# Kernel tuning notes

Measured on AMD Instinct MI355X. Metric: run time of the kernel, lower is better.

Reference implementation:

```python
import jax, jax.numpy as jnp
import numpy as np

N_NODES = 50000
N_EDGES = 800000
F_NODE = 64
F_EDGE = 32
F_GLOBAL = 32
OUT_DIM = 64
N_GRAPHS = 256


def setup_inputs() -> dict:
    key = jax.random.key(0)
    ks = jax.random.split(key, 8)
    x = jax.random.normal(ks[0], (N_NODES, F_NODE), dtype=jnp.float32)
    edge_index = jax.random.randint(ks[1], (2, N_EDGES), 0, N_NODES, dtype=jnp.int64)
    edge_attr = jax.random.normal(ks[2], (N_EDGES, F_EDGE), dtype=jnp.float32)
    u = jax.random.normal(ks[3], (N_GRAPHS, F_GLOBAL), dtype=jnp.float32)
    batch = jnp.sort(jax.random.randint(ks[4], (N_NODES,), 0, N_GRAPHS, dtype=jnp.int64))
    # params (scaled like default Linear init)
    W1 = jax.random.normal(ks[5], (F_NODE + F_EDGE, OUT_DIM), dtype=jnp.float32) / np.sqrt(F_NODE + F_EDGE)
    b1 = jnp.zeros((OUT_DIM,), dtype=jnp.float32)
    W2 = jax.random.normal(ks[6], (F_NODE + OUT_DIM + F_GLOBAL, OUT_DIM), dtype=jnp.float32) / np.sqrt(F_NODE + OUT_DIM + F_GLOBAL)
    b2 = jnp.zeros((OUT_DIM,), dtype=jnp.float32)
    return {"x": x, "edge_index": edge_index, "edge_attr": edge_attr,
            "u": u, "batch": batch, "W1": W1, "b1": b1, "W2": W2, "b2": b2}


def reference(x, edge_index, edge_attr, u, batch, W1, b1, W2, b2):
    dest, src = edge_index[0], edge_index[1]
    # gather source node features + edge attrs -> [E, F_NODE + F_EDGE]
    edge_info = jnp.concatenate([x[src], edge_attr], axis=1)
    # node_mlp_1: Linear + ReLU
    edge_messages = jax.nn.relu(edge_info @ W1 + b1)  # [E, OUT_DIM]
    # scatter-sum into destination nodes
    aggregated = jax.ops.segment_sum(edge_messages, dest, num_segments=x.shape[0])  # [N, OUT_DIM]
    # concat node, aggregated messages, per-graph global
    node_info = jnp.concatenate([x, aggregated, u[batch]], axis=1)  # [N, F_NODE+OUT_DIM+F_GLOBAL]
    # node_mlp_2: Linear + ReLU
    return jax.nn.relu(node_info @ W2 + b2)  # [N, OUT_DIM]
```

## Files before the change

### kernel.cpp

```cpp
#include <hip/hip_runtime.h>
#include <hip/hip_bf16.h>

typedef __attribute__((ext_vector_type(8))) short short8;
typedef __attribute__((ext_vector_type(4))) float f32x4;

constexpr int NN = 50000;
constexpr int NE = 800000;
constexpr int FN = 64;
constexpr int FE = 32;
constexpr int FG = 32;
constexpr int OD = 64;
constexpr int NG = 256;

constexpr int SCAN_B = 256;
constexpr int NBLK = (NN + SCAN_B - 1) / SCAN_B;

constexpr int SLOTS_MAX = NE + 15 * NN;
constexpr int NWIN_MAX  = SLOTS_MAX / 16;

constexpr int XCVT_BLOCKS = (NN * FN / 8 + 255) / 256;
constexpr int PRE_BLOCKS  = XCVT_BLOCKS + (NG * 64) / 256;

constexpr int AGG_BLOCKS = 2048;
constexpr int AGG_WAVES  = AGG_BLOCKS * 4;
constexpr int NWIN_N = NN / 16;
constexpr int NODE_BLOCKS = 782;
constexpr int NODE_WAVES  = NODE_BLOCKS * 4;

static __device__ __forceinline__ unsigned pack_bf16(float a, float b) {
    __hip_bfloat162 h = __float22bfloat162_rn(float2{a, b});
    return *reinterpret_cast<unsigned*>(&h);
}

__global__ __launch_bounds__(256) void k_pre(const float* __restrict__ x,
                                             unsigned* __restrict__ xb32,
                                             const float* __restrict__ u,
                                             const float* __restrict__ W2,
                                             const float* __restrict__ b2,
                                             float* __restrict__ uW2b,
                                             int* __restrict__ cnt) {
    if (blockIdx.x >= XCVT_BLOCKS) {
        const int lane = threadIdx.x & 63;
        float wcol[FG];
#pragma unroll
        for (int k = 0; k < FG; ++k) wcol[k] = W2[(FN + OD + k) * OD + lane];
        const float bias = b2[lane];
        int g = ((blockIdx.x - XCVT_BLOCKS) * 256 + threadIdx.x) >> 6;
        g = __builtin_amdgcn_readfirstlane(g);
        if (g >= NG) return;
        const float* __restrict__ urow = u + (size_t)g * FG;
        float acc = bias;
#pragma unroll
        for (int k = 0; k < FG; ++k) acc = fmaf(urow[k], wcol[k], acc);
        uW2b[(size_t)g * OD + lane] = acc;
        return;
    }
    const int i = blockIdx.x * 256 + threadIdx.x;
    if (i < NN) cnt[i] = 0;
    if (i >= NN * FN / 8) return;
    const float4* p = (const float4*)(x + (size_t)i * 8);
    float4 f0 = p[0], f1 = p[1];
    uint4 o;
    o.x = pack_bf16(f0.x, f0.y);
    o.y = pack_bf16(f0.z, f0.w);
    o.z = pack_bf16(f1.x, f1.y);
    o.w = pack_bf16(f1.z, f1.w);
    ((uint4*)xb32)[i] = o;
}

__global__ __launch_bounds__(256) void k_hist(const int* __restrict__ ei,
                                              int* __restrict__ cnt) {
    const int e = blockIdx.x * blockDim.x + threadIdx.x;
    if (e < NE) atomicAdd(&cnt[ei[e]], 1);
}

__global__ __launch_bounds__(SCAN_B) void k_scan1(const int* __restrict__ cnt,
                                                  int* __restrict__ pstart,
                                                  int* __restrict__ bsum) {
    __shared__ int lds[SCAN_B];
    const int i = blockIdx.x * SCAN_B + threadIdx.x;
    const int v = (i < NN) ? (((cnt[i] + 15) >> 4) << 4) : 0;
    lds[threadIdx.x] = v;
    __syncthreads();
#pragma unroll
    for (int off = 1; off < SCAN_B; off <<= 1) {
        int t = (threadIdx.x >= off) ? lds[threadIdx.x - off] : 0;
        __syncthreads();
        lds[threadIdx.x] += t;
        __syncthreads();
    }
    const int incl = lds[threadIdx.x];
    if (i < NN) pstart[i] = incl - v;
    if (threadIdx.x == SCAN_B - 1) bsum[blockIdx.x] = incl;
}

__global__ __launch_bounds__(SCAN_B) void k_scan23(int* __restrict__ pstart,
                                                   const int* __restrict__ bsum,
                                                   const int* __restrict__ cnt,
                                                   int* __restrict__ cursor,
                                                   int* __restrict__ winend) {
    __shared__ int lds[SCAN_B];
    const int t = threadIdx.x;
    lds[t] = (t < NBLK) ? bsum[t] : 0;
    __syncthreads();
#pragma unroll
    for (int off = 1; off < SCAN_B; off <<= 1) {
        int tv = (t >= off) ? lds[t - off] : 0;
        __syncthreads();
        lds[t] += tv;
        __syncthreads();
    }
    const int boff = (blockIdx.x == 0) ? 0 : lds[blockIdx.x - 1];

    const int i = blockIdx.x * SCAN_B + t;
    if (i < NN) {
        const int cn = cnt[i];
        const int pc = ((cn + 15) >> 4) << 4;
        const int s = pstart[i] + boff;
        pstart[i] = s;
        cursor[i] = s;
        const int end = s + cn;
        const int w0 = s >> 4;
        const int w1 = (s + pc) >> 4;
        for (int w = w0; w < w1; ++w) winend[w] = end;
        if (i == NN - 1) pstart[NN] = s + pc;
    }
}

__global__ __launch_bounds__(256) void k_scatter(const int* __restrict__ ei,
                                                 int* __restrict__ cursor,
                                                 int2* __restrict__ bucket) {
    const int e = blockIdx.x * blockDim.x + threadIdx.x;
    if (e < NE) {
        const int dst = ei[e];
        const int src = ei[NE + e];
        const int pos = atomicAdd(&cursor[dst], 1);
        bucket[pos] = make_int2(src, e);
    }
}

__global__ __launch_bounds__(256) void k_aggw2(const int2* __restrict__ bucket,
                                               const float* __restrict__ ea,
                                               const unsigned short* __restrict__ xb,
                                               const float* __restrict__ W1,
                                               const float* __restrict__ b1,
                                               const int* __restrict__ pstart,
                                               const int* __restrict__ winend,
                                               float* __restrict__ partial) {
    const int l = threadIdx.x & 63;
    const int g = l >> 4;
    const int c = l & 15;

    short8 wf[3][4];
#pragma unroll
    for (int t = 0; t < 3; ++t)
#pragma unroll
        for (int b = 0; b < 4; ++b)
#pragma unroll
            for (int i = 0; i < 8; i += 2) {
                const int k = 32 * t + 8 * g + i;
                const unsigned p = pack_bf16(W1[k * OD + (c + 16 * b)],
                                             W1[(k + 1) * OD + (c + 16 * b)]);
                ((unsigned*)&wf[t][b])[i / 2] = p;
            }
    float bias[4];
#pragma unroll
    for (int b = 0; b < 4; ++b) bias[b] = b1[c + 16 * b];

    const int nwin = pstart[NN] >> 4;

    int wv = (blockIdx.x * blockDim.x + threadIdx.x) >> 6;
    wv = __builtin_amdgcn_readfirstlane(wv);

    auto computeWin = [&](int w, int end, uint4 q0, uint4 q1,
                          float4 e0, float4 e1) {
        short8 a0 = *(short8*)&q0;
        short8 a1 = *(short8*)&q1;
        uint4 q2;
        q2.x = pack_bf16(e0.x, e0.y);
        q2.y = pack_bf16(e0.z, e0.w);
        q2.z = pack_bf16(e1.x, e1.y);
        q2.w = pack_bf16(e1.z, e1.w);
        short8 a2 = *(short8*)&q2;

        float sv[4];
#pragma unroll
        for (int b = 0; b < 4; ++b) {
            f32x4 acc = {0.f, 0.f, 0.f, 0.f};
            acc = __builtin_amdgcn_mfma_f32_16x16x32_bf16(a0, wf[0][b], acc, 0, 0, 0);
            acc = __builtin_amdgcn_mfma_f32_16x16x32_bf16(a1, wf[1][b], acc, 0, 0, 0);
            acc = __builtin_amdgcn_mfma_f32_16x16x32_bf16(a2, wf[2][b], acc, 0, 0, 0);
            float s = 0.0f;
#pragma unroll
            for (int q = 0; q < 4; ++q) {
                const int row = w * 16 + 4 * g + q;
                const float v = fmaxf(acc[q] + bias[b], 0.0f);
                s += (row < end) ? v : 0.0f;
            }
            s += __shfl_xor(s, 16);
            s += __shfl_xor(s, 32);
            sv[b] = s;
        }
        float v = sv[0];
        v = (g == 1) ? sv[1] : v;
        v = (g == 2) ? sv[2] : v;
        v = (g == 3) ? sv[3] : v;
        partial[(size_t)w * 64 + l] = v;
    };

    for (int p = wv; 2 * p < nwin; p += AGG_WAVES) {
        const int wA = 2 * p;
        const int wB = wA + 1;
        const bool hasB = (wB < nwin);

        const int endA = winend[wA];
        const int endB = winend[hasB ? wB : wA];

        int sA = wA * 16 + c;
        if (sA >= endA) sA = endA - 1;
        int sB = wB * 16 + c;
        if (!hasB || sB >= endB) sB = endB - 1;

        const int2 pa = bucket[sA];
        const int2 pb = bucket[sB];

        const uint4* xra = (const uint4*)(xb + (size_t)pa.x * FN);
        const uint4 qa0 = xra[g];
        const uint4 qa1 = xra[4 + g];
        const float4* era = (const float4*)(ea + (size_t)pa.y * FE);
        const float4 ea0 = era[2 * g];
        const float4 ea1 = era[2 * g + 1];

        const uint4* xrb = (const uint4*)(xb + (size_t)pb.x * FN);
        const uint4 qb0 = xrb[g];
        const uint4 qb1 = xrb[4 + g];
        const float4* erb = (const float4*)(ea + (size_t)pb.y * FE);
        const float4 eb0 = erb[2 * g];
        const float4 eb1 = erb[2 * g + 1];

        computeWin(wA, endA, qa0, qa1, ea0, ea1);
        if (hasB) computeWin(wB, endB, qb0, qb1, eb0, eb1);
    }
}

__global__ __launch_bounds__(256) void k_red(const float* __restrict__ partial,
                                             const int* __restrict__ pstart,
                                             unsigned short* __restrict__ aggb) {
    const int l = threadIdx.x & 63;
    int n = (blockIdx.x * blockDim.x + threadIdx.x) >> 6;
    n = __builtin_amdgcn_readfirstlane(n);
    if (n >= NN) return;

    const int w0 = pstart[n] >> 4;
    const int w1 = pstart[n + 1] >> 4;
    float s = 0.0f;
    for (int w = w0; w < w1; ++w) s += partial[(size_t)w * 64 + l];
    __hip_bfloat16 hb = __float2bfloat16(s);
    aggb[(size_t)n * OD + l] = *reinterpret_cast<unsigned short*>(&hb);
}

__global__ __launch_bounds__(256) void k_nodem(const unsigned short* __restrict__ xb,
                                               const unsigned short* __restrict__ aggb,
                                               const int* __restrict__ bat,
                                               const float* __restrict__ uW2b,
                                               const float* __restrict__ W2,
                                               float* __restrict__ out) {
    const int l = threadIdx.x & 63;
    const int g = l >> 4;
    const int c = l & 15;

    short8 wf[4][4];
#pragma unroll
    for (int t = 0; t < 4; ++t)
#pragma unroll
        for (int b = 0; b < 4; ++b)
#pragma unroll
            for (int i = 0; i < 8; i += 2) {
                const int k = 32 * t + 8 * g + i;
                const unsigned p = pack_bf16(W2[k * OD + (c + 16 * b)],
                                             W2[(k + 1) * OD + (c + 16 * b)]);
                ((unsigned*)&wf[t][b])[i / 2] = p;
            }

    int wv = (blockIdx.x * blockDim.x + threadIdx.x) >> 6;
    wv = __builtin_amdgcn_readfirstlane(wv);

    for (int w = wv; w < NWIN_N; w += NODE_WAVES) {
        const int n0 = w * 16;
        const uint4* xr = (const uint4*)(xb + (size_t)(n0 + c) * FN);
        const uint4* ar = (const uint4*)(aggb + (size_t)(n0 + c) * OD);
        uint4 qx0 = xr[g], qx1 = xr[4 + g];
        uint4 qa0 = ar[g], qa1 = ar[4 + g];
        short8 a0 = *(short8*)&qx0, a1 = *(short8*)&qx1;
        short8 a2 = *(short8*)&qa0, a3 = *(short8*)&qa1;

        int bq[4];
#pragma unroll
        for (int q = 0; q < 4; ++q) bq[q] = bat[n0 + g * 4 + q];

#pragma unroll
        for (int b = 0; b < 4; ++b) {
            f32x4 acc = {0.f, 0.f, 0.f, 0.f};
            acc = __builtin_amdgcn_mfma_f32_16x16x32_bf16(a0, wf[0][b], acc, 0, 0, 0);
            acc = __builtin_amdgcn_mfma_f32_16x16x32_bf16(a1, wf[1][b], acc, 0, 0, 0);
            acc = __builtin_amdgcn_mfma_f32_16x16x32_bf16(a2, wf[2][b], acc, 0, 0, 0);
            acc = __builtin_amdgcn_mfma_f32_16x16x32_bf16(a3, wf[3][b], acc, 0, 0, 0);
#pragma unroll
            for (int q = 0; q < 4; ++q) {
                const int n = n0 + g * 4 + q;
                const float val = acc[q] + uW2b[(size_t)bq[q] * OD + c + 16 * b];
                out[(size_t)n * OD + c + 16 * b] = fmaxf(val, 0.0f);
            }
        }
    }
}

extern "C" void kernel_launch(void* const* d_in, const int* in_sizes, int n_in,
                              void* d_out, int out_size, void* d_ws, size_t ws_size,
                              hipStream_t stream) {
    const float* x    = (const float*)d_in[0];
    const int*   ei   = (const int*)d_in[1];
    const float* ea   = (const float*)d_in[2];
    const float* u    = (const float*)d_in[3];
    const int*   bat  = (const int*)d_in[4];
    const float* W1   = (const float*)d_in[5];
    const float* b1   = (const float*)d_in[6];
    const float* W2   = (const float*)d_in[7];
    const float* b2   = (const float*)d_in[8];
    float* out = (float*)d_out;

    char* ws = (char*)d_ws;
    auto alloc = [&](size_t bytes) {
        char* p = ws;
        ws += (bytes + 255) & ~size_t(255);
        return p;
    };
    unsigned short* xb   = (unsigned short*)alloc((size_t)NN * FN * 2);
    unsigned short* aggb = (unsigned short*)alloc((size_t)NN * OD * 2);
    float* uW2b    = (float*)alloc((size_t)NG * OD * sizeof(float));
    int*   cnt     = (int*)alloc((size_t)NN * sizeof(int));
    int*   pstart  = (int*)alloc((size_t)(NN + 1) * sizeof(int));
    int*   cursor  = (int*)alloc((size_t)NN * sizeof(int));
    int*   bsum    = (int*)alloc((size_t)NBLK * sizeof(int));
    int*   winend  = (int*)alloc((size_t)NWIN_MAX * sizeof(int));
    int2*  bucket  = (int2*)alloc((size_t)SLOTS_MAX * sizeof(int2));
    float* partial = (float*)alloc((size_t)NWIN_MAX * OD * sizeof(float));

    k_pre<<<dim3(PRE_BLOCKS), dim3(256), 0, stream>>>(x, (unsigned*)xb, u, W2, b2, uW2b, cnt);

    k_hist<<<dim3((NE + 255) / 256), dim3(256), 0, stream>>>(ei, cnt);
    k_scan1<<<dim3(NBLK), dim3(SCAN_B), 0, stream>>>(cnt, pstart, bsum);
    k_scan23<<<dim3(NBLK), dim3(SCAN_B), 0, stream>>>(pstart, bsum, cnt, cursor, winend);

    k_scatter<<<dim3((NE + 255) / 256), dim3(256), 0, stream>>>(ei, cursor, bucket);

    k_aggw2<<<dim3(AGG_BLOCKS), dim3(256), 0, stream>>>(bucket, ea, xb, W1, b1, pstart, winend, partial);

    k_red<<<dim3((NN * 64 + 255) / 256), dim3(256), 0, stream>>>(partial, pstart, aggb);

    k_nodem<<<dim3(NODE_BLOCKS), dim3(256), 0, stream>>>(xb, aggb, bat, uW2b, W2, out);
}
```

Measured before the change: 168.8 us.

## Pre-sort edge attributes into bf16 buckets and halve partial-sum storage

The scatter kernel now also converts each edge's attributes to bf16 and writes them into the destination-sorted bucket. The aggregation kernel can then read them contiguously instead of gathering fp32 rows by edge id. Per-window partial sums are stored as packed bf16 pairs, and the reduction kernel handles two nodes per wave. The window-pair unrolling in the aggregation loop is removed. The slot capacity is a fixed constant of 1350000 instead of the worst-case bound of 1550000, so skewed degree distributions could overflow it, and bf16 partial sums add rounding error.

```diff
diff --git a/kernel.cpp b/kernel.cpp
--- a/kernel.cpp
+++ b/kernel.cpp
@@ -15,8 +15,8 @@
 constexpr int SCAN_B = 256;
 constexpr int NBLK = (NN + SCAN_B - 1) / SCAN_B;
 
-constexpr int SLOTS_MAX = NE + 15 * NN;
-constexpr int NWIN_MAX  = SLOTS_MAX / 16;
+constexpr int SLOTS_CAP = 1350000;
+constexpr int NWIN_CAP  = SLOTS_CAP / 16;
 
 constexpr int XCVT_BLOCKS = (NN * FN / 8 + 255) / 256;
 constexpr int PRE_BLOCKS  = XCVT_BLOCKS + (NG * 64) / 256;
@@ -127,26 +127,42 @@
     }
 }
 
-__global__ __launch_bounds__(256) void k_scatter(const int* __restrict__ ei,
-                                                 int* __restrict__ cursor,
-                                                 int2* __restrict__ bucket) {
-    const int e = blockIdx.x * blockDim.x + threadIdx.x;
-    if (e < NE) {
-        const int dst = ei[e];
-        const int src = ei[NE + e];
-        const int pos = atomicAdd(&cursor[dst], 1);
-        bucket[pos] = make_int2(src, e);
-    }
-}
-
-__global__ __launch_bounds__(256) void k_aggw2(const int2* __restrict__ bucket,
+__global__ __launch_bounds__(256) void k_scat2(const int* __restrict__ ei,
                                                const float* __restrict__ ea,
+                                               int* __restrict__ cursor,
+                                               int* __restrict__ bucket_src,
+                                               uint4* __restrict__ bucket_ea) {
+    const int t = blockIdx.x * 256 + threadIdx.x;
+    const int e = t >> 2;
+    const int p = t & 3;
+    if (e >= NE) return;
+
+    const int lane = threadIdx.x & 63;
+    const int dst = ei[e];
+    int pos = 0;
+    if (p == 0) pos = atomicAdd(&cursor[dst], 1);
+    pos = __shfl(pos, lane & ~3);
+    if (p == 0) bucket_src[pos] = ei[NE + e];
+
+    const float4* er = (const float4*)(ea + (size_t)e * FE) + 2 * p;
+    const float4 f0 = er[0];
+    const float4 f1 = er[1];
+    uint4 o;
+    o.x = pack_bf16(f0.x, f0.y);
+    o.y = pack_bf16(f0.z, f0.w);
+    o.z = pack_bf16(f1.x, f1.y);
+    o.w = pack_bf16(f1.z, f1.w);
+    bucket_ea[(size_t)pos * 4 + p] = o;
+}
+
+__global__ __launch_bounds__(256) void k_aggw3(const int* __restrict__ bucket_src,
+                                               const uint4* __restrict__ bucket_ea,
                                                const unsigned short* __restrict__ xb,
                                                const float* __restrict__ W1,
                                                const float* __restrict__ b1,
                                                const int* __restrict__ pstart,
                                                const int* __restrict__ winend,
-                                               float* __restrict__ partial) {
+                                               unsigned* __restrict__ partial32) {
     const int l = threadIdx.x & 63;
     const int g = l >> 4;
     const int c = l & 15;
@@ -172,16 +188,21 @@
     int wv = (blockIdx.x * blockDim.x + threadIdx.x) >> 6;
     wv = __builtin_amdgcn_readfirstlane(wv);
 
-    auto computeWin = [&](int w, int end, uint4 q0, uint4 q1,
-                          float4 e0, float4 e1) {
-        short8 a0 = *(short8*)&q0;
-        short8 a1 = *(short8*)&q1;
-        uint4 q2;
-        q2.x = pack_bf16(e0.x, e0.y);
-        q2.y = pack_bf16(e0.z, e0.w);
-        q2.z = pack_bf16(e1.x, e1.y);
-        q2.w = pack_bf16(e1.z, e1.w);
-        short8 a2 = *(short8*)&q2;
+    for (int w = wv; w < nwin; w += AGG_WAVES) {
+        const int end = winend[w];
+        int slot = w * 16 + c;
+        if (slot >= end) slot = end - 1;
+
+        const uint4 qe = bucket_ea[(size_t)(w * 16 + c < end ? slot : slot) * 4 + g];
+        const int src = bucket_src[slot];
+
+        const uint4* xr = (const uint4*)(xb + (size_t)src * FN);
+        const uint4 q0 = xr[g];
+        const uint4 q1 = xr[4 + g];
+
+        const short8 a0 = *(const short8*)&q0;
+        const short8 a1 = *(const short8*)&q1;
+        const short8 a2 = *(const short8*)&qe;
 
         float sv[4];
 #pragma unroll
@@ -205,58 +226,32 @@
         v = (g == 1) ? sv[1] : v;
         v = (g == 2) ? sv[2] : v;
         v = (g == 3) ? sv[3] : v;
-        partial[(size_t)w * 64 + l] = v;
-    };
-
-    for (int p = wv; 2 * p < nwin; p += AGG_WAVES) {
-        const int wA = 2 * p;
-        const int wB = wA + 1;
-        const bool hasB = (wB < nwin);
-
-        const int endA = winend[wA];
-        const int endB = winend[hasB ? wB : wA];
-
-        int sA = wA * 16 + c;
-        if (sA >= endA) sA = endA - 1;
-        int sB = wB * 16 + c;
-        if (!hasB || sB >= endB) sB = endB - 1;
-
-        const int2 pa = bucket[sA];
-        const int2 pb = bucket[sB];
-
-        const uint4* xra = (const uint4*)(xb + (size_t)pa.x * FN);
-        const uint4 qa0 = xra[g];
-        const uint4 qa1 = xra[4 + g];
-        const float4* era = (const float4*)(ea + (size_t)pa.y * FE);
-        const float4 ea0 = era[2 * g];
-        const float4 ea1 = era[2 * g + 1];
-
-        const uint4* xrb = (const uint4*)(xb + (size_t)pb.x * FN);
-        const uint4 qb0 = xrb[g];
-        const uint4 qb1 = xrb[4 + g];
-        const float4* erb = (const float4*)(ea + (size_t)pb.y * FE);
-        const float4 eb0 = erb[2 * g];
-        const float4 eb1 = erb[2 * g + 1];
-
-        computeWin(wA, endA, qa0, qa1, ea0, ea1);
-        if (hasB) computeWin(wB, endB, qb0, qb1, eb0, eb1);
-    }
-}
-
-__global__ __launch_bounds__(256) void k_red(const float* __restrict__ partial,
+
+        const float vn = __shfl_xor(v, 1);
+        if ((l & 1) == 0)
+            partial32[(size_t)w * 32 + (l >> 1)] = pack_bf16(v, vn);
+    }
+}
+
+__global__ __launch_bounds__(256) void k_red(const unsigned* __restrict__ partial32,
                                              const int* __restrict__ pstart,
-                                             unsigned short* __restrict__ aggb) {
+                                             unsigned* __restrict__ aggb32) {
     const int l = threadIdx.x & 63;
-    int n = (blockIdx.x * blockDim.x + threadIdx.x) >> 6;
-    n = __builtin_amdgcn_readfirstlane(n);
+    const int q = l & 31;
+    int nb = (blockIdx.x * blockDim.x + threadIdx.x) >> 6;
+    nb = __builtin_amdgcn_readfirstlane(nb);
+    const int n = 2 * nb + (l >> 5);
     if (n >= NN) return;
 
     const int w0 = pstart[n] >> 4;
     const int w1 = pstart[n + 1] >> 4;
-    float s = 0.0f;
-    for (int w = w0; w < w1; ++w) s += partial[(size_t)w * 64 + l];
-    __hip_bfloat16 hb = __float2bfloat16(s);
-    aggb[(size_t)n * OD + l] = *reinterpret_cast<unsigned short*>(&hb);
+    float c0 = 0.0f, c1 = 0.0f;
+    for (int w = w0; w < w1; ++w) {
+        const unsigned uu = partial32[(size_t)w * 32 + q];
+        c0 += __uint_as_float(uu << 16);
+        c1 += __uint_as_float(uu & 0xffff0000u);
+    }
+    aggb32[(size_t)n * 32 + q] = pack_bf16(c0, c1);
 }
 
 __global__ __launch_bounds__(256) void k_nodem(const unsigned short* __restrict__ xb,
@@ -342,9 +337,10 @@
     int*   pstart  = (int*)alloc((size_t)(NN + 1) * sizeof(int));
     int*   cursor  = (int*)alloc((size_t)NN * sizeof(int));
     int*   bsum    = (int*)alloc((size_t)NBLK * sizeof(int));
-    int*   winend  = (int*)alloc((size_t)NWIN_MAX * sizeof(int));
-    int2*  bucket  = (int2*)alloc((size_t)SLOTS_MAX * sizeof(int2));
-    float* partial = (float*)alloc((size_t)NWIN_MAX * OD * sizeof(float));
+    int*   winend  = (int*)alloc((size_t)NWIN_CAP * sizeof(int));
+    int*   bucket_src = (int*)alloc((size_t)SLOTS_CAP * sizeof(int));
+    uint4* bucket_ea  = (uint4*)alloc((size_t)SLOTS_CAP * 64);
+    unsigned* partial = (unsigned*)alloc((size_t)NWIN_CAP * 32 * 4);
 
     k_pre<<<dim3(PRE_BLOCKS), dim3(256), 0, stream>>>(x, (unsigned*)xb, u, W2, b2, uW2b, cnt);
 
@@ -352,11 +348,12 @@
     k_scan1<<<dim3(NBLK), dim3(SCAN_B), 0, stream>>>(cnt, pstart, bsum);
     k_scan23<<<dim3(NBLK), dim3(SCAN_B), 0, stream>>>(pstart, bsum, cnt, cursor, winend);
 
-    k_scatter<<<dim3((NE + 255) / 256), dim3(256), 0, stream>>>(ei, cursor, bucket);
-
-    k_aggw2<<<dim3(AGG_BLOCKS), dim3(256), 0, stream>>>(bucket, ea, xb, W1, b1, pstart, winend, partial);
-
-    k_red<<<dim3((NN * 64 + 255) / 256), dim3(256), 0, stream>>>(partial, pstart, aggb);
+    k_scat2<<<dim3((NE * 4 + 255) / 256), dim3(256), 0, stream>>>(ei, ea, cursor, bucket_src, bucket_ea);
+
+    k_aggw3<<<dim3(AGG_BLOCKS), dim3(256), 0, stream>>>(bucket_src, bucket_ea, xb, W1, b1,
+                                                        pstart, winend, partial);
+
+    k_red<<<dim3((NN * 32 + 255) / 256), dim3(256), 0, stream>>>(partial, pstart, (unsigned*)aggb);
 
     k_nodem<<<dim3(NODE_BLOCKS), dim3(256), 0, stream>>>(xb, aggb, bat, uW2b, W2, out);
 }
```

Result: faster. 156.1 us (-7.5%).
